# Optimization experiments

Measured on AMD Instinct MI355X. Metric: run time of the kernel, lower is better.

The kernel has to match this reference:

```python
import jax, jax.numpy as jnp
import numpy as np

N, E = 50000, 800000
DIN, DEIN, H, FN, FE = 128, 32, 4, 16, 16
NEG_SLOPE = 0.2


def setup_inputs() -> dict:
    key = jax.random.key(0)
    ks = jax.random.split(key, 10)
    nfeats = jax.random.normal(ks[0], (N, DIN), jnp.float32)
    efeats = jax.random.normal(ks[1], (E, DEIN), jnp.float32)
    src = jax.random.randint(ks[2], (E,), 0, N)
    dst = jax.random.randint(ks[3], (E,), 0, N)
    s = 0.1  # xavier-ish scale
    W_ni = jax.random.normal(ks[4], (DIN, H * FE), jnp.float32) * s
    W_nj = jax.random.normal(ks[5], (DIN, H * FE), jnp.float32) * s
    W_fij = jax.random.normal(ks[6], (DEIN, H * FE), jnp.float32) * s
    W_node = jax.random.normal(ks[7], (DIN, H * FN), jnp.float32) * s
    attn = jax.random.normal(ks[8], (1, H, FE), jnp.float32) * s
    bias = jnp.zeros((H * FE,), jnp.float32)
    return {"nfeats": nfeats, "efeats": efeats, "W_ni": W_ni, "W_nj": W_nj,
            "W_fij": W_fij, "W_node": W_node, "attn": attn, "bias": bias,
            "src": src, "dst": dst}


def reference(nfeats, efeats, W_ni, W_nj, W_fij, W_node, attn, bias, src, dst):
    n = nfeats.shape[0]
    h, fe = attn.shape[1], attn.shape[2]
    # node-side edge-feature projections
    f_ni = nfeats @ W_ni          # [N, H*FE]
    f_nj = nfeats @ W_nj          # [N, H*FE]
    f_fij = efeats @ W_fij        # [E, H*FE]
    # u_add_v gather + edge feature + bias, then leaky relu
    f_out = jax.nn.leaky_relu(f_ni[src] + f_nj[dst] + f_fij + bias, NEG_SLOPE)
    f_out = f_out.reshape(-1, h, fe)                      # [E, H, FE]
    e = jnp.sum(f_out * attn, axis=-1)                    # [E, H] attention logits
    # edge softmax grouped by destination node (segment softmax)
    m = jax.ops.segment_max(e, dst, num_segments=n)       # [N, H]
    a = jnp.exp(e - m[dst])                               # [E, H]
    denom = jax.ops.segment_sum(a, dst, num_segments=n)   # [N, H]
    a = a / denom[dst]                                    # [E, H]
    # weighted neighbor aggregation (u_mul_e -> sum at dst)
    h_src = (nfeats @ W_node).reshape(n, h, -1)           # [N, H, FN]
    msg = h_src[src] * a[:, :, None]                      # [E, H, FN]
    h_out = jax.ops.segment_sum(msg, dst, num_segments=n) # [N, H, FN]
    return h_out.reshape(n, -1), f_out.reshape(f_out.shape[0], -1)
```

## Files before the change

kernel.cpp:

```cpp
#include <hip/hip_runtime.h>
#include <hip/hip_bf16.h>

#define NN 50000
#define NE 800000
#define DIN 128
#define DEIN 32
#define PD 192
#define NEG_SLOPE 0.2f

typedef __bf16 bf16x8 __attribute__((ext_vector_type(8)));
typedef __bf16 bf16x4 __attribute__((ext_vector_type(4)));
typedef float f32x4 __attribute__((ext_vector_type(4)));
using bf16 = __hip_bfloat16;

__device__ inline float b2f(__bf16 b) {
    unsigned short u = __builtin_bit_cast(unsigned short, b);
    return __uint_as_float((unsigned)u << 16);
}

__device__ inline bf16x8 load8_f32_to_bf16(const float* p) {
    f32x4 a = *reinterpret_cast<const f32x4*>(p);
    f32x4 b = *reinterpret_cast<const f32x4*>(p + 4);
    bf16x8 r;
#pragma unroll
    for (int j = 0; j < 4; j++) {
        r[j]     = (__bf16)a[j];
        r[j + 4] = (__bf16)b[j];
    }
    return r;
}

__device__ inline void async_copy16(const void* g, void* lds) {
    __builtin_amdgcn_global_load_lds(
        (const __attribute__((address_space(1))) void*)g,
        (__attribute__((address_space(3))) void*)lds, 16, 0, 0);
}

__global__ __launch_bounds__(512) void k_node_gemm(
    const float* __restrict__ nfeats,
    const float* __restrict__ Wni, const float* __restrict__ Wnj,
    const float* __restrict__ Wnode,
    bf16* __restrict__ P, int* __restrict__ counts)
{
    __shared__ __align__(16) __bf16 sW[192][136];
    const int t = threadIdx.x;
    const int lane = t & 63;
    const int wid  = t >> 6;
    const int lo = lane & 15, hi = lane >> 4;

    {
        int z = blockIdx.x * 512 + t;
        if (z < NN) counts[z] = 0;
    }

    const float* tabs[3] = {Wni, Wnj, Wnode};
#pragma unroll
    for (int tb = 0; tb < 3; tb++) {
#pragma unroll
        for (int q = 0; q < 4; q++) {
            int flat = t + q * 512;
            int k  = flat >> 4;
            int c4 = (flat & 15) * 4;
            f32x4 w4 = *reinterpret_cast<const f32x4*>(&tabs[tb][k * 64 + c4]);
#pragma unroll
            for (int i = 0; i < 4; i++)
                sW[tb * 64 + c4 + i][k] = (__bf16)w4[i];
        }
    }

    const int rbase = blockIdx.x * 128 + wid * 16;
    bf16x8 afrag[4];
#pragma unroll
    for (int kk = 0; kk < 4; kk++) {
        int row = rbase + lo; if (row >= NN) row = NN - 1;
        afrag[kk] = load8_f32_to_bf16(&nfeats[(size_t)row*DIN + kk*32 + hi*8]);
    }
    __syncthreads();

#pragma unroll
    for (int ct = 0; ct < 12; ct++) {
        f32x4 acc = {0.f, 0.f, 0.f, 0.f};
#pragma unroll
        for (int kk = 0; kk < 4; kk++) {
            bf16x8 bfrag = *reinterpret_cast<const bf16x8*>(&sW[ct*16 + lo][kk*32 + hi*8]);
            acc = __builtin_amdgcn_mfma_f32_16x16x32_bf16(afrag[kk], bfrag, acc, 0, 0, 0);
        }
#pragma unroll
        for (int r = 0; r < 4; r++) {
            int row = rbase + hi*4 + r;
            if (row < NN) P[(size_t)row*PD + ct*16 + lo] = __float2bfloat16(acc[r]);
        }
    }
}

__global__ void k_hist(const int* __restrict__ dst, int* __restrict__ counts, int e) {
    int i = blockIdx.x * blockDim.x + threadIdx.x;
    if (i < e) atomicAdd(&counts[dst[i]], 1);
}

__global__ __launch_bounds__(256) void k_bsum(const int* __restrict__ counts,
                                              int* __restrict__ bsum, int n) {
    __shared__ int ws[4];
    const int gid = blockIdx.x * 256 + threadIdx.x;
    const int lane = threadIdx.x & 63, wid = threadIdx.x >> 6;
    int v = (gid < n) ? counts[gid] : 0;
#pragma unroll
    for (int s = 1; s < 64; s <<= 1) v += __shfl_xor(v, s);
    if (lane == 0) ws[wid] = v;
    __syncthreads();
    if (threadIdx.x == 0) bsum[blockIdx.x] = ws[0] + ws[1] + ws[2] + ws[3];
}

__global__ __launch_bounds__(256) void k_bscan(const int* __restrict__ bsum,
                                               int* __restrict__ bpre,
                                               int* __restrict__ offsets, int nb) {
    __shared__ int ws[4];
    const int t = threadIdx.x, lane = t & 63, wid = t >> 6;
    int v = (t < nb) ? bsum[t] : 0;
    int sc = v;
#pragma unroll
    for (int s = 1; s < 64; s <<= 1) { int u = __shfl_up(sc, s); if (lane >= s) sc += u; }
    if (lane == 63) ws[wid] = sc;
    __syncthreads();
    int woff = 0;
    for (int k = 0; k < wid; k++) woff += ws[k];
    if (t < nb) bpre[t] = woff + sc - v;
    if (t == 0) offsets[NN] = NE;
}

__global__ __launch_bounds__(256) void k_apply(const int* __restrict__ counts,
                                               const int* __restrict__ bpre,
                                               int* __restrict__ offsets,
                                               int* __restrict__ cursor, int n) {
    __shared__ int ws[4];
    const int gid = blockIdx.x * 256 + threadIdx.x;
    const int t = threadIdx.x, lane = t & 63, wid = t >> 6;
    int v = (gid < n) ? counts[gid] : 0;
    int sc = v;
#pragma unroll
    for (int s = 1; s < 64; s <<= 1) { int u = __shfl_up(sc, s); if (lane >= s) sc += u; }
    if (lane == 63) ws[wid] = sc;
    __syncthreads();
    int woff = 0;
    for (int k = 0; k < wid; k++) woff += ws[k];
    const int ex = bpre[blockIdx.x] + woff + sc - v;
    if (gid < n) { offsets[gid] = ex; cursor[gid] = ex; }
}

__global__ void k_scatter(const int* __restrict__ dst, const int* __restrict__ src,
                          int* __restrict__ cursor, int* __restrict__ eidx,
                          int* __restrict__ srcp, int e) {
    int i = blockIdx.x * blockDim.x + threadIdx.x;
    if (i < e) {
        int p = atomicAdd(&cursor[dst[i]], 1);
        eidx[p] = i;
        srcp[p] = src[i];
    }
}

__global__ __launch_bounds__(512) void k_edge(
    const float* __restrict__ efeats,
    const float* __restrict__ Wf,
    const float* __restrict__ attn,
    const float* __restrict__ bias,
    const bf16* __restrict__ P,
    const int* __restrict__ src, const int* __restrict__ dst,
    float* __restrict__ f_out,
    float* __restrict__ el)
{
    __shared__ __align__(16) char smem[36864];
    __bf16* sWf = reinterpret_cast<__bf16*>(smem + 32768);
    const int t = threadIdx.x;
    const int lane = t & 63, wid = t >> 6;
    const int lo = lane & 15, hi = lane >> 4;
    const int e0w = blockIdx.x * 128 + wid * 16;
    const int c4 = (lane & 15) * 4;

    {
        int k  = t >> 4;
        int cc = (t & 15) * 4;
        f32x4 w4 = *reinterpret_cast<const f32x4*>(&Wf[k * 64 + cc]);
#pragma unroll
        for (int i = 0; i < 4; i++) sWf[(cc + i)*32 + k] = (__bf16)w4[i];
    }
    __syncthreads();

    int sd = 0;
    if (lane < 32) sd = (lane < 16) ? src[e0w + lane] : dst[e0w + lane - 16];

    __bf16* spw = reinterpret_cast<__bf16*>(smem) + wid * 2048;
#pragma unroll
    for (int q = 0; q < 4; q++) {
        const int c = lane + q * 64;
        const int table = c >> 7, row16 = (c >> 3) & 15, part = c & 7;
        const int nid = __shfl(sd, table * 16 + row16);
        const bf16* g = P + (size_t)nid * PD + table * 64 + part * 8;
        async_copy16(g, reinterpret_cast<__bf16*>(smem) + (size_t)(wid*2048 + q*512));
    }

    bf16x8 afrag = load8_f32_to_bf16(&efeats[(size_t)(e0w + lo)*DEIN + hi*8]);
    bf16x8 bfr[4];
#pragma unroll
    for (int ct = 0; ct < 4; ct++)
        bfr[ct] = *reinterpret_cast<const bf16x8*>(&sWf[(ct*16 + lo)*32 + hi*8]);

    f32x4 att4  = *reinterpret_cast<const f32x4*>(&attn[c4]);
    f32x4 bias4 = *reinterpret_cast<const f32x4*>(&bias[c4]);

    asm volatile("s_waitcnt vmcnt(0)" ::: "memory");
    __builtin_amdgcn_sched_barrier(0);

    bf16x4 pi4[4], pj4[4];
#pragma unroll
    for (int q = 0; q < 4; q++) {
        const int lrow = (lane >> 4) + q*4;
        pi4[q] = *reinterpret_cast<const bf16x4*>(&spw[lrow*64 + c4]);
        pj4[q] = *reinterpret_cast<const bf16x4*>(&spw[1024 + lrow*64 + c4]);
    }

    f32x4 accv[4];
#pragma unroll
    for (int ct = 0; ct < 4; ct++) {
        f32x4 z = {0.f, 0.f, 0.f, 0.f};
        accv[ct] = __builtin_amdgcn_mfma_f32_16x16x32_bf16(afrag, bfr[ct], z, 0, 0, 0);
    }

    float* sOutF = reinterpret_cast<float*>(smem + wid * 4096);
#pragma unroll
    for (int ct = 0; ct < 4; ct++)
#pragma unroll
        for (int r = 0; r < 4; r++)
            sOutF[(hi*4 + r)*64 + ((ct*16 + lo) ^ (hi << 4))] = accv[ct][r];

#pragma unroll
    for (int q = 0; q < 4; q++) {
        const int lrow = (lane >> 4) + q*4;
        f32x4 o = *reinterpret_cast<const f32x4*>(&sOutF[lrow*64 + (c4 ^ (q << 4))]);
        f32x4 x;
#pragma unroll
        for (int i = 0; i < 4; i++) {
            float xv = o[i] + b2f(pi4[q][i]) + b2f(pj4[q][i]) + bias4[i];
            x[i] = xv > 0.f ? xv : NEG_SLOPE * xv;
        }
        *reinterpret_cast<f32x4*>(&f_out[(size_t)(e0w + lrow)*64 + c4]) = x;
        float partial = x[0]*att4[0] + x[1]*att4[1] + x[2]*att4[2] + x[3]*att4[3];
        partial += __shfl_xor(partial, 1);
        partial += __shfl_xor(partial, 2);
        const float ev = __expf(partial);
        if ((lane & 3) == 0)
            el[(size_t)(e0w + lrow)*4 + ((lane & 15) >> 2)] = ev;
    }
}

__global__ __launch_bounds__(256) void k_aggregate(
    const int* __restrict__ offsets, const int* __restrict__ eidx,
    const int* __restrict__ srcp, const float* __restrict__ el,
    const bf16* __restrict__ P, float* __restrict__ h_out)
{
    const int lane = threadIdx.x & 63;
    const int wid  = threadIdx.x >> 6;
    const int n = blockIdx.x * 4 + wid;
    if (n >= NN) return;
    const int off0 = offsets[n], off1 = offsets[n + 1];
    const int h4 = lane & 3;
    const int slot4 = lane >> 2;

    float denp = 0.f, acc = 0.f;
    for (int c0 = off0; c0 < off1; c0 += 16) {
        const int cnt = off1 - c0;
        float a_ld = 0.f;
        int s_ld = 0;
        if (slot4 < cnt) {
            const int e = eidx[c0 + slot4];
            a_ld = el[(size_t)e*4 + h4];
            s_ld = srcp[c0 + slot4];
        }
        denp += a_ld;
#pragma unroll
        for (int q = 0; q < 16; q++) {
            const float wq = __shfl(a_ld, (q << 2) | (lane >> 4));
            const int   sq = __shfl(s_ld, q << 2);
            acc += wq * __bfloat162float(P[(size_t)sq*PD + 128 + lane]);
        }
    }
    denp += __shfl_xor(denp, 4);
    denp += __shfl_xor(denp, 8);
    denp += __shfl_xor(denp, 16);
    denp += __shfl_xor(denp, 32);
    const float den = __shfl(denp, lane >> 4);
    h_out[(size_t)n*64 + lane] = (off1 > off0) ? acc / den : 0.f;
}

extern "C" void kernel_launch(void* const* d_in, const int* in_sizes, int n_in,
                              void* d_out, int out_size, void* d_ws, size_t ws_size,
                              hipStream_t stream) {
    const float* nfeats = (const float*)d_in[0];
    const float* efeats = (const float*)d_in[1];
    const float* Wni    = (const float*)d_in[2];
    const float* Wnj    = (const float*)d_in[3];
    const float* Wfij   = (const float*)d_in[4];
    const float* Wnode  = (const float*)d_in[5];
    const float* attn   = (const float*)d_in[6];
    const float* bias   = (const float*)d_in[7];
    const int*   src    = (const int*)d_in[8];
    const int*   dst    = (const int*)d_in[9];

    float* h_out = (float*)d_out;
    float* f_out = (float*)d_out + (size_t)NN * 64;

    char* ws = (char*)d_ws;
    size_t off = 0;
    auto carve = [&](size_t bytes) -> void* {
        void* p = ws + off;
        off = (off + bytes + 255) & ~(size_t)255;
        return p;
    };
    const int NB = (NN + 255) / 256;
    bf16*  P       = (bf16*) carve((size_t)NN * PD * sizeof(bf16));
    float* el      = (float*)carve((size_t)NE * 4 * sizeof(float));
    int*   counts  = (int*)  carve((size_t)NN * sizeof(int));
    int*   cursor  = (int*)  carve((size_t)NN * sizeof(int));
    int*   offsets = (int*)  carve((size_t)(NN + 1) * sizeof(int));
    int*   eidx    = (int*)  carve((size_t)NE * sizeof(int));
    int*   srcp    = (int*)  carve((size_t)NE * sizeof(int));
    int*   bsum    = (int*)  carve((size_t)NB * sizeof(int));
    int*   bpre    = (int*)  carve((size_t)NB * sizeof(int));
    (void)ws_size; (void)in_sizes; (void)n_in; (void)out_size;

    hipLaunchKernelGGL(k_node_gemm, dim3((NN + 127) / 128), dim3(512), 0, stream,
                       nfeats, Wni, Wnj, Wnode, P, counts);
    hipLaunchKernelGGL(k_hist, dim3((NE + 255) / 256), dim3(256), 0, stream,
                       dst, counts, NE);
    hipLaunchKernelGGL(k_bsum, dim3(NB), dim3(256), 0, stream, counts, bsum, NN);
    hipLaunchKernelGGL(k_bscan, dim3(1), dim3(256), 0, stream, bsum, bpre, offsets, NB);
    hipLaunchKernelGGL(k_apply, dim3(NB), dim3(256), 0, stream,
                       counts, bpre, offsets, cursor, NN);
    hipLaunchKernelGGL(k_scatter, dim3((NE + 255) / 256), dim3(256), 0, stream,
                       dst, src, cursor, eidx, srcp, NE);
    hipLaunchKernelGGL(k_edge, dim3(NE / 128), dim3(512), 0, stream,
                       efeats, Wfij, attn, bias, P, src, dst, f_out, el);
    hipLaunchKernelGGL(k_aggregate, dim3((NN + 3) / 4), dim3(256), 0, stream,
                       offsets, eidx, srcp, el, P, h_out);
}
```

Measured before the change: 227.7 us.

## Swap MFMA operand order to drop LDS staging in edge kernel

```diff
diff --git a/kernel.cpp b/kernel.cpp
--- a/kernel.cpp
+++ b/kernel.cpp
@@ -28,12 +28,6 @@
         r[j + 4] = (__bf16)b[j];
     }
     return r;
-}
-
-__device__ inline void async_copy16(const void* g, void* lds) {
-    __builtin_amdgcn_global_load_lds(
-        (const __attribute__((address_space(1))) void*)g,
-        (__attribute__((address_space(3))) void*)lds, 16, 0, 0);
 }
 
 __global__ __launch_bounds__(512) void k_node_gemm(
@@ -69,10 +63,11 @@
     }
 
     const int rbase = blockIdx.x * 128 + wid * 16;
+    const int myrow = rbase + lo;
     bf16x8 afrag[4];
 #pragma unroll
     for (int kk = 0; kk < 4; kk++) {
-        int row = rbase + lo; if (row >= NN) row = NN - 1;
+        int row = myrow >= NN ? NN - 1 : myrow;
         afrag[kk] = load8_f32_to_bf16(&nfeats[(size_t)row*DIN + kk*32 + hi*8]);
     }
     __syncthreads();
@@ -83,13 +78,13 @@
 #pragma unroll
         for (int kk = 0; kk < 4; kk++) {
             bf16x8 bfrag = *reinterpret_cast<const bf16x8*>(&sW[ct*16 + lo][kk*32 + hi*8]);
-            acc = __builtin_amdgcn_mfma_f32_16x16x32_bf16(afrag[kk], bfrag, acc, 0, 0, 0);
-        }
-#pragma unroll
-        for (int r = 0; r < 4; r++) {
-            int row = rbase + hi*4 + r;
-            if (row < NN) P[(size_t)row*PD + ct*16 + lo] = __float2bfloat16(acc[r]);
-        }
+            acc = __builtin_amdgcn_mfma_f32_16x16x32_bf16(bfrag, afrag[kk], acc, 0, 0, 0);
+        }
+        bf16x4 pk;
+#pragma unroll
+        for (int r = 0; r < 4; r++) pk[r] = (__bf16)acc[r];
+        if (myrow < NN)
+            *reinterpret_cast<bf16x4*>(&P[(size_t)myrow*PD + ct*16 + hi*4]) = pk;
     }
 }
 
@@ -168,87 +163,70 @@
     float* __restrict__ f_out,
     float* __restrict__ el)
 {
-    __shared__ __align__(16) char smem[36864];
-    __bf16* sWf = reinterpret_cast<__bf16*>(smem + 32768);
+    __shared__ __align__(16) __bf16 sWf[64][32];
     const int t = threadIdx.x;
     const int lane = t & 63, wid = t >> 6;
     const int lo = lane & 15, hi = lane >> 4;
     const int e0w = blockIdx.x * 128 + wid * 16;
-    const int c4 = (lane & 15) * 4;
+    const int myedge = e0w + lo;
 
     {
         int k  = t >> 4;
         int cc = (t & 15) * 4;
         f32x4 w4 = *reinterpret_cast<const f32x4*>(&Wf[k * 64 + cc]);
 #pragma unroll
-        for (int i = 0; i < 4; i++) sWf[(cc + i)*32 + k] = (__bf16)w4[i];
-    }
-    __syncthreads();
-
-    int sd = 0;
-    if (lane < 32) sd = (lane < 16) ? src[e0w + lane] : dst[e0w + lane - 16];
-
-    __bf16* spw = reinterpret_cast<__bf16*>(smem) + wid * 2048;
-#pragma unroll
-    for (int q = 0; q < 4; q++) {
-        const int c = lane + q * 64;
-        const int table = c >> 7, row16 = (c >> 3) & 15, part = c & 7;
-        const int nid = __shfl(sd, table * 16 + row16);
-        const bf16* g = P + (size_t)nid * PD + table * 64 + part * 8;
-        async_copy16(g, reinterpret_cast<__bf16*>(smem) + (size_t)(wid*2048 + q*512));
-    }
-
-    bf16x8 afrag = load8_f32_to_bf16(&efeats[(size_t)(e0w + lo)*DEIN + hi*8]);
+        for (int i = 0; i < 4; i++) sWf[cc + i][k] = (__bf16)w4[i];
+    }
+
+    bf16x8 afrag = load8_f32_to_bf16(&efeats[(size_t)myedge*DEIN + hi*8]);
+
+    const int si = src[myedge];
+    const int di = dst[myedge];
+    bf16x4 pi[4], pj[4];
+#pragma unroll
+    for (int ct = 0; ct < 4; ct++) {
+        pi[ct] = *reinterpret_cast<const bf16x4*>(&P[(size_t)si*PD + ct*16 + hi*4]);
+        pj[ct] = *reinterpret_cast<const bf16x4*>(&P[(size_t)di*PD + 64 + ct*16 + hi*4]);
+    }
+
+    f32x4 att4[4], bias4[4];
+#pragma unroll
+    for (int ct = 0; ct < 4; ct++) {
+        att4[ct]  = *reinterpret_cast<const f32x4*>(&attn[ct*16 + hi*4]);
+        bias4[ct] = *reinterpret_cast<const f32x4*>(&bias[ct*16 + hi*4]);
+    }
+
+    __syncthreads();
+
     bf16x8 bfr[4];
 #pragma unroll
     for (int ct = 0; ct < 4; ct++)
-        bfr[ct] = *reinterpret_cast<const bf16x8*>(&sWf[(ct*16 + lo)*32 + hi*8]);
-
-    f32x4 att4  = *reinterpret_cast<const f32x4*>(&attn[c4]);
-    f32x4 bias4 = *reinterpret_cast<const f32x4*>(&bias[c4]);
-
-    asm volatile("s_waitcnt vmcnt(0)" ::: "memory");
-    __builtin_amdgcn_sched_barrier(0);
-
-    bf16x4 pi4[4], pj4[4];
-#pragma unroll
-    for (int q = 0; q < 4; q++) {
-        const int lrow = (lane >> 4) + q*4;
-        pi4[q] = *reinterpret_cast<const bf16x4*>(&spw[lrow*64 + c4]);
-        pj4[q] = *reinterpret_cast<const bf16x4*>(&spw[1024 + lrow*64 + c4]);
-    }
-
-    f32x4 accv[4];
+        bfr[ct] = *reinterpret_cast<const bf16x8*>(&sWf[ct*16 + lo][hi*8]);
+
+    float ve0, ve1, ve2, ve3;
 #pragma unroll
     for (int ct = 0; ct < 4; ct++) {
         f32x4 z = {0.f, 0.f, 0.f, 0.f};
-        accv[ct] = __builtin_amdgcn_mfma_f32_16x16x32_bf16(afrag, bfr[ct], z, 0, 0, 0);
-    }
-
-    float* sOutF = reinterpret_cast<float*>(smem + wid * 4096);
-#pragma unroll
-    for (int ct = 0; ct < 4; ct++)
-#pragma unroll
-        for (int r = 0; r < 4; r++)
-            sOutF[(hi*4 + r)*64 + ((ct*16 + lo) ^ (hi << 4))] = accv[ct][r];
-
-#pragma unroll
-    for (int q = 0; q < 4; q++) {
-        const int lrow = (lane >> 4) + q*4;
-        f32x4 o = *reinterpret_cast<const f32x4*>(&sOutF[lrow*64 + (c4 ^ (q << 4))]);
+        f32x4 d = __builtin_amdgcn_mfma_f32_16x16x32_bf16(bfr[ct], afrag, z, 0, 0, 0);
         f32x4 x;
 #pragma unroll
         for (int i = 0; i < 4; i++) {
-            float xv = o[i] + b2f(pi4[q][i]) + b2f(pj4[q][i]) + bias4[i];
+            float xv = d[i] + b2f(pi[ct][i]) + b2f(pj[ct][i]) + bias4[ct][i];
             x[i] = xv > 0.f ? xv : NEG_SLOPE * xv;
         }
-        *reinterpret_cast<f32x4*>(&f_out[(size_t)(e0w + lrow)*64 + c4]) = x;
-        float partial = x[0]*att4[0] + x[1]*att4[1] + x[2]*att4[2] + x[3]*att4[3];
-        partial += __shfl_xor(partial, 1);
-        partial += __shfl_xor(partial, 2);
-        const float ev = __expf(partial);
-        if ((lane & 3) == 0)
-            el[(size_t)(e0w + lrow)*4 + ((lane & 15) >> 2)] = ev;
+        *reinterpret_cast<f32x4*>(&f_out[(size_t)myedge*64 + ct*16 + hi*4]) = x;
+        float partial = x[0]*att4[ct][0] + x[1]*att4[ct][1]
+                      + x[2]*att4[ct][2] + x[3]*att4[ct][3];
+        partial += __shfl_xor(partial, 16);
+        partial += __shfl_xor(partial, 32);
+        if (ct == 0) ve0 = partial;
+        else if (ct == 1) ve1 = partial;
+        else if (ct == 2) ve2 = partial;
+        else ve3 = partial;
+    }
+    if (hi == 0) {
+        f32x4 ev = { __expf(ve0), __expf(ve1), __expf(ve2), __expf(ve3) };
+        *reinterpret_cast<f32x4*>(&el[(size_t)myedge*4]) = ev;
     }
 }
 
```

New measurement: 256.4 us. 12.6% more time.

## Fuse CSR build into one cooperative kernel with grid syncs

Applied to the files above, without the earlier changes.

```diff
diff --git a/kernel.cpp b/kernel.cpp
--- a/kernel.cpp
+++ b/kernel.cpp
@@ -1,5 +1,8 @@
 #include <hip/hip_runtime.h>
 #include <hip/hip_bf16.h>
+#include <hip/hip_cooperative_groups.h>
+
+namespace cg = cooperative_groups;
 
 #define NN 50000
 #define NE 800000
@@ -7,6 +10,8 @@
 #define DEIN 32
 #define PD 192
 #define NEG_SLOPE 0.2f
+#define CSR_NB 196
+#define CSR_GRID 512
 
 typedef __bf16 bf16x8 __attribute__((ext_vector_type(8)));
 typedef __bf16 bf16x4 __attribute__((ext_vector_type(4)));
@@ -93,65 +98,65 @@
     }
 }
 
-__global__ void k_hist(const int* __restrict__ dst, int* __restrict__ counts, int e) {
-    int i = blockIdx.x * blockDim.x + threadIdx.x;
-    if (i < e) atomicAdd(&counts[dst[i]], 1);
-}
-
-__global__ __launch_bounds__(256) void k_bsum(const int* __restrict__ counts,
-                                              int* __restrict__ bsum, int n) {
+__global__ __launch_bounds__(256) void k_csr(
+    const int* __restrict__ dst, const int* __restrict__ src,
+    int* __restrict__ counts, int* __restrict__ offsets,
+    int* __restrict__ cursor, int* __restrict__ eidx,
+    int* __restrict__ srcp, int* __restrict__ bsum)
+{
+    cg::grid_group grid = cg::this_grid();
+    const int t = threadIdx.x;
+    const int b = blockIdx.x;
+    const int gid = b * 256 + t;
+    const int gsz = CSR_GRID * 256;
+    const int lane = t & 63, wid = t >> 6;
     __shared__ int ws[4];
-    const int gid = blockIdx.x * 256 + threadIdx.x;
-    const int lane = threadIdx.x & 63, wid = threadIdx.x >> 6;
-    int v = (gid < n) ? counts[gid] : 0;
-#pragma unroll
-    for (int s = 1; s < 64; s <<= 1) v += __shfl_xor(v, s);
-    if (lane == 0) ws[wid] = v;
-    __syncthreads();
-    if (threadIdx.x == 0) bsum[blockIdx.x] = ws[0] + ws[1] + ws[2] + ws[3];
-}
-
-__global__ __launch_bounds__(256) void k_bscan(const int* __restrict__ bsum,
-                                               int* __restrict__ bpre,
-                                               int* __restrict__ offsets, int nb) {
-    __shared__ int ws[4];
-    const int t = threadIdx.x, lane = t & 63, wid = t >> 6;
-    int v = (t < nb) ? bsum[t] : 0;
-    int sc = v;
-#pragma unroll
-    for (int s = 1; s < 64; s <<= 1) { int u = __shfl_up(sc, s); if (lane >= s) sc += u; }
-    if (lane == 63) ws[wid] = sc;
-    __syncthreads();
-    int woff = 0;
-    for (int k = 0; k < wid; k++) woff += ws[k];
-    if (t < nb) bpre[t] = woff + sc - v;
-    if (t == 0) offsets[NN] = NE;
-}
-
-__global__ __launch_bounds__(256) void k_apply(const int* __restrict__ counts,
-                                               const int* __restrict__ bpre,
-                                               int* __restrict__ offsets,
-                                               int* __restrict__ cursor, int n) {
-    __shared__ int ws[4];
-    const int gid = blockIdx.x * 256 + threadIdx.x;
-    const int t = threadIdx.x, lane = t & 63, wid = t >> 6;
-    int v = (gid < n) ? counts[gid] : 0;
-    int sc = v;
-#pragma unroll
-    for (int s = 1; s < 64; s <<= 1) { int u = __shfl_up(sc, s); if (lane >= s) sc += u; }
-    if (lane == 63) ws[wid] = sc;
-    __syncthreads();
-    int woff = 0;
-    for (int k = 0; k < wid; k++) woff += ws[k];
-    const int ex = bpre[blockIdx.x] + woff + sc - v;
-    if (gid < n) { offsets[gid] = ex; cursor[gid] = ex; }
-}
-
-__global__ void k_scatter(const int* __restrict__ dst, const int* __restrict__ src,
-                          int* __restrict__ cursor, int* __restrict__ eidx,
-                          int* __restrict__ srcp, int e) {
-    int i = blockIdx.x * blockDim.x + threadIdx.x;
-    if (i < e) {
+    __shared__ int sbp;
+
+    for (int i = gid; i < NE; i += gsz)
+        atomicAdd(&counts[dst[i]], 1);
+    grid.sync();
+
+    if (b < CSR_NB) {
+        int v = (gid < NN) ? counts[gid] : 0;
+        int s = v;
+#pragma unroll
+        for (int sh = 1; sh < 64; sh <<= 1) s += __shfl_xor(s, sh);
+        if (lane == 0) ws[wid] = s;
+        __syncthreads();
+        if (t == 0) bsum[b] = ws[0] + ws[1] + ws[2] + ws[3];
+    }
+    grid.sync();
+
+    if (b < CSR_NB) {
+        int bv = (t < CSR_NB) ? bsum[t] : 0;
+        int bs = bv;
+#pragma unroll
+        for (int sh = 1; sh < 64; sh <<= 1) { int u = __shfl_up(bs, sh); if (lane >= sh) bs += u; }
+        __syncthreads();
+        if (lane == 63) ws[wid] = bs;
+        __syncthreads();
+        int woffb = 0;
+        for (int k = 0; k < wid; k++) woffb += ws[k];
+        if (t == b) sbp = woffb + bs - bv;
+        __syncthreads();
+        const int bpre_b = sbp;
+
+        int v = (gid < NN) ? counts[gid] : 0;
+        int sc = v;
+#pragma unroll
+        for (int sh = 1; sh < 64; sh <<= 1) { int u = __shfl_up(sc, sh); if (lane >= sh) sc += u; }
+        if (lane == 63) ws[wid] = sc;
+        __syncthreads();
+        int woff = 0;
+        for (int k = 0; k < wid; k++) woff += ws[k];
+        const int ex = bpre_b + woff + sc - v;
+        if (gid < NN) { offsets[gid] = ex; cursor[gid] = ex; }
+    }
+    if (gid == 0) offsets[NN] = NE;
+    grid.sync();
+
+    for (int i = gid; i < NE; i += gsz) {
         int p = atomicAdd(&cursor[dst[i]], 1);
         eidx[p] = i;
         srcp[p] = src[i];
@@ -278,9 +283,11 @@
         denp += a_ld;
 #pragma unroll
         for (int q = 0; q < 16; q++) {
-            const float wq = __shfl(a_ld, (q << 2) | (lane >> 4));
-            const int   sq = __shfl(s_ld, q << 2);
-            acc += wq * __bfloat162float(P[(size_t)sq*PD + 128 + lane]);
+            if (q < cnt) {
+                const float wq = __shfl(a_ld, (q << 2) | (lane >> 4));
+                const int   sq = __shfl(s_ld, q << 2);
+                acc += wq * __bfloat162float(P[(size_t)sq*PD + 128 + lane]);
+            }
         }
     }
     denp += __shfl_xor(denp, 4);
@@ -315,7 +322,6 @@
         off = (off + bytes + 255) & ~(size_t)255;
         return p;
     };
-    const int NB = (NN + 255) / 256;
     bf16*  P       = (bf16*) carve((size_t)NN * PD * sizeof(bf16));
     float* el      = (float*)carve((size_t)NE * 4 * sizeof(float));
     int*   counts  = (int*)  carve((size_t)NN * sizeof(int));
@@ -323,20 +329,19 @@
     int*   offsets = (int*)  carve((size_t)(NN + 1) * sizeof(int));
     int*   eidx    = (int*)  carve((size_t)NE * sizeof(int));
     int*   srcp    = (int*)  carve((size_t)NE * sizeof(int));
-    int*   bsum    = (int*)  carve((size_t)NB * sizeof(int));
-    int*   bpre    = (int*)  carve((size_t)NB * sizeof(int));
+    int*   bsum    = (int*)  carve((size_t)256 * sizeof(int));
     (void)ws_size; (void)in_sizes; (void)n_in; (void)out_size;
 
     hipLaunchKernelGGL(k_node_gemm, dim3((NN + 127) / 128), dim3(512), 0, stream,
                        nfeats, Wni, Wnj, Wnode, P, counts);
-    hipLaunchKernelGGL(k_hist, dim3((NE + 255) / 256), dim3(256), 0, stream,
-                       dst, counts, NE);
-    hipLaunchKernelGGL(k_bsum, dim3(NB), dim3(256), 0, stream, counts, bsum, NN);
-    hipLaunchKernelGGL(k_bscan, dim3(1), dim3(256), 0, stream, bsum, bpre, offsets, NB);
-    hipLaunchKernelGGL(k_apply, dim3(NB), dim3(256), 0, stream,
-                       counts, bpre, offsets, cursor, NN);
-    hipLaunchKernelGGL(k_scatter, dim3((NE + 255) / 256), dim3(256), 0, stream,
-                       dst, src, cursor, eidx, srcp, NE);
+
+    {
+        void* args[] = { (void*)&dst, (void*)&src, (void*)&counts, (void*)&offsets,
+                         (void*)&cursor, (void*)&eidx, (void*)&srcp, (void*)&bsum };
+        hipLaunchCooperativeKernel((const void*)k_csr, dim3(CSR_GRID), dim3(256),
+                                   args, 0, stream);
+    }
+
     hipLaunchKernelGGL(k_edge, dim3(NE / 128), dim3(512), 0, stream,
                        efeats, Wfij, attn, bias, P, src, dst, f_out, el);
     hipLaunchKernelGGL(k_aggregate, dim3((NN + 3) / 4), dim3(256), 0, stream,
```

After: 421.0 us. +84.9%, slower.
